# Kernel optimization log

Hardware: AMD Instinct MI355X
Metric: run time of the kernel (lower is better)

The kernel has to match this reference:

```python
import jax, jax.numpy as jnp
import numpy as np


def setup_inputs() -> dict:
    key = jax.random.key(0)
    k1, k2, k3 = jax.random.split(key, 3)
    B, T, C = 4, 2048, 1024
    x = jax.random.normal(k1, (B, T, C), dtype=jnp.float32)
    # Linear weights stored as (in, out) so y = x @ W + b
    w_attn = jax.random.normal(k2, (C, 3 * C), dtype=jnp.float32) * (1.0 / np.sqrt(C))
    b_attn = jnp.zeros((3 * C,), dtype=jnp.float32)
    w_proj = jax.random.normal(k3, (C, C), dtype=jnp.float32) * (1.0 / np.sqrt(C))
    b_proj = jnp.zeros((C,), dtype=jnp.float32)
    return {"x": x, "w_attn": w_attn, "b_attn": b_attn, "w_proj": w_proj, "b_proj": b_proj}


def reference(x, w_attn, b_attn, w_proj, b_proj):
    B, T, C = x.shape
    n_head = 16
    hd = C // n_head  # head dim = 64
    qkv = x @ w_attn + b_attn  # [B, T, 3C]
    q, k, v = jnp.split(qkv, 3, axis=-1)
    # [B, H, T, hd]
    q = q.reshape(B, T, n_head, hd).transpose(0, 2, 1, 3)
    k = k.reshape(B, T, n_head, hd).transpose(0, 2, 1, 3)
    v = v.reshape(B, T, n_head, hd).transpose(0, 2, 1, 3)
    scale = 1.0 / np.sqrt(hd).astype(np.float32)
    att = jnp.einsum("bhqd,bhkd->bhqk", q, k) * scale  # [B, H, T, T]
    causal = jnp.tril(jnp.ones((T, T), dtype=bool))
    att = jnp.where(causal[None, None], att, jnp.float32(-jnp.inf))
    att = jax.nn.softmax(att, axis=-1)
    y = jnp.einsum("bhqk,bhkd->bhqd", att, v)  # [B, H, T, hd]
    y = y.transpose(0, 2, 1, 3).reshape(B, T, C)
    return y @ w_proj + b_proj
```

## Files before the change

kernel.cpp:

```cpp
#include <hip/hip_runtime.h>

typedef __attribute__((ext_vector_type(8))) short short8;
typedef __attribute__((ext_vector_type(4))) float f32x4;
typedef unsigned short u16;
typedef unsigned int u32;

__device__ __forceinline__ float bf2f(u16 u) {
    union { u32 i; float f; } x;
    x.i = ((u32)u) << 16;
    return x.f;
}

__device__ __forceinline__ u16 f2bf(float f) {
    union { float f; u32 i; } x;
    x.f = f;
    u32 r = x.i + 0x7fffu + ((x.i >> 16) & 1u);
    return (u16)(r >> 16);
}

__global__ __launch_bounds__(256) void convert_bf16(const float* __restrict__ in,
                                                    u16* __restrict__ out) {
    const long i = ((long)blockIdx.x * 256 + threadIdx.x) * 8;
    f32x4 v0 = *(const f32x4*)(in + i);
    f32x4 v1 = *(const f32x4*)(in + i + 4);
    short8 o;
#pragma unroll
    for (int j = 0; j < 4; ++j) o[j] = (short)f2bf(v0[j]);
#pragma unroll
    for (int j = 0; j < 4; ++j) o[4 + j] = (short)f2bf(v1[j]);
    *(short8*)(out + i) = o;
}

__global__ __launch_bounds__(256) void transpose_f32_bf16(const float* __restrict__ in,
                                                          u16* __restrict__ out,
                                                          int K, int N) {
    __shared__ float tile[32][33];
    const int nb = blockIdx.x * 32, kb = blockIdx.y * 32;
    const int tx = threadIdx.x, ty = threadIdx.y;
#pragma unroll
    for (int i = 0; i < 32; i += 8)
        tile[ty + i][tx] = in[(long)(kb + ty + i) * N + nb + tx];
    __syncthreads();
#pragma unroll
    for (int i = 0; i < 32; i += 8)
        out[(long)(nb + ty + i) * K + kb + tx] = f2bf(tile[tx][ty + i]);
}

__global__ __launch_bounds__(256) void transpose_v(const u16* __restrict__ qkv,
                                                   u16* __restrict__ vT) {
    __shared__ u16 tile[32][33];
    const int tb = blockIdx.x * 32;
    const int db = blockIdx.y * 32;
    const int bh = blockIdx.z;
    const int b = bh >> 4, h = bh & 15;
    const int tx = threadIdx.x, ty = threadIdx.y;
#pragma unroll
    for (int i = 0; i < 32; i += 8)
        tile[ty + i][tx] = qkv[((long)b * 2048 + tb + ty + i) * 3072 + 2048 + h * 64 + db + tx];
    __syncthreads();
#pragma unroll
    for (int i = 0; i < 32; i += 8)
        vT[((long)bh * 64 + db + ty + i) * 2048 + tb + tx] = tile[tx][ty + i];
}

__global__ __launch_bounds__(256, 2) void gemm_bf16_bt(
    const u16* __restrict__ A, int lda, const u16* __restrict__ BT,
    const float* __restrict__ bias, u16* __restrict__ C,
    int M, int N, int K) {
    __shared__ u16 As[128 * 32];
    __shared__ u16 Bs[128 * 32];
    const int tid = threadIdx.x;
    const int wv = tid >> 6, lane = tid & 63, quad = lane >> 4, L = lane & 15;
    const int wm = (wv >> 1) * 64, wn = (wv & 1) * 64;
    const long m0 = (long)blockIdx.y * 128;
    const long n0 = (long)blockIdx.x * 128;

    const u16* Ag = A + (m0 + wv * 32 + (lane >> 2)) * (long)lda + (lane & 3) * 8;
    const u16* Bg = BT + (n0 + wv * 32 + (lane >> 2)) * (long)K + (lane & 3) * 8;
    u16* AsW = &As[wv * 32 * 32];
    u16* BsW = &Bs[wv * 32 * 32];

    f32x4 zero4 = {0.f, 0.f, 0.f, 0.f};
    f32x4 acc[4][4];
#pragma unroll
    for (int i = 0; i < 4; ++i)
#pragma unroll
        for (int j = 0; j < 4; ++j) acc[i][j] = zero4;

    for (int kb = 0; kb < K; kb += 32) {
        short8 a0 = *(const short8*)(Ag + kb);
        short8 a1 = *(const short8*)(Ag + kb + (long)16 * lda);
        short8 b0 = *(const short8*)(Bg + kb);
        short8 b1 = *(const short8*)(Bg + kb + (long)16 * K);
        __syncthreads();
        *(short8*)(AsW + lane * 8) = a0;
        *(short8*)(AsW + 512 + lane * 8) = a1;
        *(short8*)(BsW + lane * 8) = b0;
        *(short8*)(BsW + 512 + lane * 8) = b1;
        __syncthreads();

        short8 af[4], bf[4];
#pragma unroll
        for (int mt = 0; mt < 4; ++mt)
            af[mt] = *(const short8*)&As[(wm + mt * 16 + L) * 32 + quad * 8];
#pragma unroll
        for (int nt = 0; nt < 4; ++nt)
            bf[nt] = *(const short8*)&Bs[(wn + nt * 16 + L) * 32 + quad * 8];
#pragma unroll
        for (int mt = 0; mt < 4; ++mt)
#pragma unroll
            for (int nt = 0; nt < 4; ++nt)
                acc[mt][nt] = __builtin_amdgcn_mfma_f32_16x16x32_bf16(
                    af[mt], bf[nt], acc[mt][nt], 0, 0, 0);
    }

#pragma unroll
    for (int nt = 0; nt < 4; ++nt) {
        const long col = n0 + wn + nt * 16 + L;
        const float bv = bias[col];
#pragma unroll
        for (int mt = 0; mt < 4; ++mt)
#pragma unroll
            for (int r = 0; r < 4; ++r) {
                const long row = m0 + wm + mt * 16 + quad * 4 + r;
                C[row * N + col] = f2bf(acc[mt][nt][r] + bv);
            }
    }
}

__global__ __launch_bounds__(256, 2) void gemm_bf16_bn(
    const u16* __restrict__ A, int lda, const float* __restrict__ B,
    const float* __restrict__ bias, float* __restrict__ C,
    int M, int N, int K) {
    __shared__ u16 As[128 * 32];
    __shared__ u16 Bs[128 * 32];
    const int tid = threadIdx.x;
    const int wv = tid >> 6, lane = tid & 63, quad = lane >> 4, L = lane & 15;
    const int wm = (wv >> 1) * 64, wn = (wv & 1) * 64;
    const long m0 = (long)blockIdx.y * 128;
    const long n0 = (long)blockIdx.x * 128;

    const u16* Ag = A + (m0 + wv * 32 + (lane >> 2)) * (long)lda + (lane & 3) * 8;
    u16* AsW = &As[wv * 32 * 32];

    f32x4 zero4 = {0.f, 0.f, 0.f, 0.f};
    f32x4 acc[4][4];
#pragma unroll
    for (int i = 0; i < 4; ++i)
#pragma unroll
        for (int j = 0; j < 4; ++j) acc[i][j] = zero4;

    for (int kb = 0; kb < K; kb += 32) {
        short8 a0 = *(const short8*)(Ag + kb);
        short8 a1 = *(const short8*)(Ag + kb + (long)16 * lda);
        short8 p[2];
#pragma unroll
        for (int i = 0; i < 2; ++i) {
            const int c = tid + i * 256;
            const int n = c >> 2, k8 = (c & 3) * 8;
            const float* bp = B + (long)(kb + k8) * N + n0 + n;
#pragma unroll
            for (int j = 0; j < 8; ++j) p[i][j] = (short)f2bf(bp[(long)j * N]);
        }
        __syncthreads();
        *(short8*)(AsW + lane * 8) = a0;
        *(short8*)(AsW + 512 + lane * 8) = a1;
        *(short8*)(&Bs[tid * 8]) = p[0];
        *(short8*)(&Bs[(tid + 256) * 8]) = p[1];
        __syncthreads();

        short8 af[4], bf[4];
#pragma unroll
        for (int mt = 0; mt < 4; ++mt)
            af[mt] = *(const short8*)&As[(wm + mt * 16 + L) * 32 + quad * 8];
#pragma unroll
        for (int nt = 0; nt < 4; ++nt)
            bf[nt] = *(const short8*)&Bs[(wn + nt * 16 + L) * 32 + quad * 8];
#pragma unroll
        for (int mt = 0; mt < 4; ++mt)
#pragma unroll
            for (int nt = 0; nt < 4; ++nt)
                acc[mt][nt] = __builtin_amdgcn_mfma_f32_16x16x32_bf16(
                    af[mt], bf[nt], acc[mt][nt], 0, 0, 0);
    }

#pragma unroll
    for (int nt = 0; nt < 4; ++nt) {
        const long col = n0 + wn + nt * 16 + L;
        const float bv = bias[col];
#pragma unroll
        for (int mt = 0; mt < 4; ++mt)
#pragma unroll
            for (int r = 0; r < 4; ++r) {
                const long row = m0 + wm + mt * 16 + quad * 4 + r;
                C[row * N + col] = acc[mt][nt][r] + bv;
            }
    }
}

#define AT_T 2048

__global__ __launch_bounds__(256) void attn_kernel(u16* __restrict__ qkv,
                                                   const u16* __restrict__ vT) {
    __shared__ u16 Kt[2][32 * 72];
    __shared__ u16 Vt[2][64 * 40];
    __shared__ u16 Ps[4][16 * 72];
    const int tid = threadIdx.x;
    const int wv = tid >> 6, lane = tid & 63, quad = lane >> 4, L = lane & 15;
    const int bh = blockIdx.x;
    const int b = bh >> 4, h = bh & 15;
    const long rowbase = (long)b * AT_T;
    const long cbase = (long)h * 64;

    const int krow = tid >> 3, kc = tid & 7;
    const int vrow = tid >> 2, vc = tid & 3;
    const u16* Kg = qkv + (rowbase + krow) * 3072 + 1024 + cbase + kc * 8;
    const u16* Vg = vT + ((long)bh * 64 + vrow) * 2048 + vc * 8;

    short8 ones;
#pragma unroll
    for (int j = 0; j < 8; ++j) ones[j] = (L == 0) ? (short)0x3F80 : (short)0;

    f32x4 zero4 = {0.f, 0.f, 0.f, 0.f};
    u16* PsW = Ps[wv];

    for (int pass = 0; pass < 2; ++pass) {
        const int qtile = (pass == 0) ? (31 - (int)blockIdx.y) : (int)blockIdx.y;
        const int q0 = qtile * 64;
        const int qw0 = q0 + wv * 16;
        const int nkb = 2 * qtile + 2;

        short8 qf[2];
#pragma unroll
        for (int s = 0; s < 2; ++s)
            qf[s] = *(const short8*)&qkv[(rowbase + qw0 + L) * 3072 + cbase + s * 32 + quad * 8];

        f32x4 accO[4], accL = zero4;
#pragma unroll
        for (int nt = 0; nt < 4; ++nt) accO[nt] = zero4;

        {
            short8 k0r = *(const short8*)Kg;
            short8 v0r = *(const short8*)Vg;
            *(short8*)&Kt[0][krow * 72 + kc * 8] = k0r;
            *(short8*)&Vt[0][vrow * 40 + vc * 8] = v0r;
        }
        __syncthreads();

        int p = 0;
        for (int kb = 0; kb < nkb; ++kb) {
            const int k0 = kb * 32;
            const bool more = (kb + 1) < nkb;
            short8 knx, vnx;
            if (more) {
                knx = *(const short8*)(Kg + (long)(k0 + 32) * 3072);
                vnx = *(const short8*)(Vg + k0 + 32);
            }

            if (k0 <= qw0 + 15) {
                f32x4 sA[2];
#pragma unroll
                for (int nt = 0; nt < 2; ++nt) {
                    short8 kf0 = *(const short8*)&Kt[p][(nt * 16 + L) * 72 + quad * 8];
                    short8 kf1 = *(const short8*)&Kt[p][(nt * 16 + L) * 72 + 32 + quad * 8];
                    f32x4 z = __builtin_amdgcn_mfma_f32_16x16x32_bf16(qf[0], kf0, zero4, 0, 0, 0);
                    sA[nt] = __builtin_amdgcn_mfma_f32_16x16x32_bf16(qf[1], kf1, z, 0, 0, 0);
                }
                if (k0 + 31 > qw0) {
#pragma unroll
                    for (int nt = 0; nt < 2; ++nt) {
                        const int key = k0 + nt * 16 + L;
#pragma unroll
                        for (int r = 0; r < 4; ++r) {
                            const int qq = qw0 + quad * 4 + r;
                            const float v = (key <= qq) ? fmaf(sA[nt][r], 0.125f, -20.0f) : -1e30f;
                            PsW[(quad * 4 + r) * 72 + nt * 16 + L] =
                                (u16)(__float_as_uint(__expf(v)) >> 16);
                        }
                    }
                } else {
#pragma unroll
                    for (int nt = 0; nt < 2; ++nt)
#pragma unroll
                        for (int r = 0; r < 4; ++r) {
                            const float pv = __expf(fmaf(sA[nt][r], 0.125f, -20.0f));
                            PsW[(quad * 4 + r) * 72 + nt * 16 + L] =
                                (u16)(__float_as_uint(pv) >> 16);
                        }
                }
                short8 pf = *(const short8*)&PsW[L * 72 + quad * 8];
                accL = __builtin_amdgcn_mfma_f32_16x16x32_bf16(pf, ones, accL, 0, 0, 0);
#pragma unroll
                for (int nt = 0; nt < 4; ++nt) {
                    short8 vf = *(const short8*)&Vt[p][(nt * 16 + L) * 40 + quad * 8];
                    accO[nt] = __builtin_amdgcn_mfma_f32_16x16x32_bf16(pf, vf, accO[nt], 0, 0, 0);
                }
            }

            if (more) {
                *(short8*)&Kt[p ^ 1][krow * 72 + kc * 8] = knx;
                *(short8*)&Vt[p ^ 1][vrow * 40 + vc * 8] = vnx;
            }
            __syncthreads();
            p ^= 1;
        }

#pragma unroll
        for (int r = 0; r < 4; ++r) {
            const float l = __shfl(accL[r], lane & 48);
            const float inv = 1.f / l;
            const long orow = (rowbase + qw0 + quad * 4 + r) * 3072 + cbase;
#pragma unroll
            for (int nt = 0; nt < 4; ++nt)
                qkv[orow + nt * 16 + L] = f2bf(accO[nt][r] * inv);
        }
    }
}

extern "C" void kernel_launch(void* const* d_in, const int* in_sizes, int n_in,
                              void* d_out, int out_size, void* d_ws, size_t ws_size,
                              hipStream_t stream) {
    const float* x      = (const float*)d_in[0];
    const float* w_attn = (const float*)d_in[1];
    const float* b_attn = (const float*)d_in[2];
    const float* w_proj = (const float*)d_in[3];
    const float* b_proj = (const float*)d_in[4];
    float* out = (float*)d_out;

    u16* qkv = (u16*)d_ws;
    u16* xb  = (u16*)d_out;
    u16* wTa = (u16*)((char*)d_out + 16777216);
    u16* vT  = (u16*)d_out;

    convert_bf16<<<4096, 256, 0, stream>>>(x, xb);
    transpose_f32_bf16<<<dim3(3072 / 32, 1024 / 32), dim3(32, 8), 0, stream>>>(
        w_attn, wTa, 1024, 3072);
    gemm_bf16_bt<<<dim3(3072 / 128, 8192 / 128), 256, 0, stream>>>(
        xb, 1024, wTa, b_attn, qkv, 8192, 3072, 1024);
    transpose_v<<<dim3(64, 2, 64), dim3(32, 8), 0, stream>>>(qkv, vT);
    attn_kernel<<<dim3(64, 16), 256, 0, stream>>>(qkv, vT);
    gemm_bf16_bn<<<dim3(1024 / 128, 8192 / 128), 256, 0, stream>>>(
        qkv, 3072, w_proj, b_proj, out, 8192, 1024, 1024);
}
```

Measured before the change: 296.6 us.

## Use 32x32x16 MFMA with register-resident P in attention kernel

The attention kernel moves from 16x16x32 to 32x32x16 MFMA tiles and computes S transposed (K as the A operand), so each lane already holds probabilities in the layout the PV MFMA needs. P is packed with v_cvt_pk_bf16 and rearranged with permlane32 swaps instead of a round trip through shared memory, and exp is computed with exp2 using pre-folded constants. Query tiles grow to 128 rows with 32 rows per wave, which halves the grid. The cost is coarser causal-skip granularity, fewer blocks, and higher register pressure from the 16-wide accumulators.

```diff
diff --git a/kernel.cpp b/kernel.cpp
--- a/kernel.cpp
+++ b/kernel.cpp
@@ -2,6 +2,7 @@
 
 typedef __attribute__((ext_vector_type(8))) short short8;
 typedef __attribute__((ext_vector_type(4))) float f32x4;
+typedef __attribute__((ext_vector_type(16))) float f32x16;
 typedef unsigned short u16;
 typedef unsigned int u32;
 
@@ -17,6 +18,32 @@
     u32 r = x.i + 0x7fffu + ((x.i >> 16) & 1u);
     return (u16)(r >> 16);
 }
+
+__device__ __forceinline__ u32 cvt_pk_bf16(float lo, float hi) {
+    u32 d;
+    asm("v_cvt_pk_bf16_f32 %0, %1, %2" : "=v"(d) : "v"(lo), "v"(hi));
+    return d;
+}
+
+__device__ __forceinline__ void pswap(u32& a, u32& b) {
+#if __has_builtin(__builtin_amdgcn_permlane32_swap)
+    auto r = __builtin_amdgcn_permlane32_swap(a, b, false, false);
+    a = r[0];
+    b = r[1];
+#else
+    const int l = (int)(threadIdx.x & 63);
+    const u32 ax = __shfl(a, l ^ 32);
+    const u32 bx = __shfl(b, l ^ 32);
+    a = (l < 32) ? a : bx;
+    b = (l < 32) ? ax : b;
+#endif
+}
+
+#if __has_builtin(__builtin_amdgcn_exp2f)
+#define EXP2F(x) __builtin_amdgcn_exp2f(x)
+#else
+#define EXP2F(x) exp2f(x)
+#endif
 
 __global__ __launch_bounds__(256) void convert_bf16(const float* __restrict__ in,
                                                     u16* __restrict__ out) {
@@ -204,9 +231,9 @@
                                                    const u16* __restrict__ vT) {
     __shared__ u16 Kt[2][32 * 72];
     __shared__ u16 Vt[2][64 * 40];
-    __shared__ u16 Ps[4][16 * 72];
     const int tid = threadIdx.x;
-    const int wv = tid >> 6, lane = tid & 63, quad = lane >> 4, L = lane & 15;
+    const int wv = tid >> 6, lane = tid & 63;
+    const int hi = lane >> 5, cc = lane & 31;
     const int bh = blockIdx.x;
     const int b = bh >> 4, h = bh & 15;
     const long rowbase = (long)b * AT_T;
@@ -219,25 +246,25 @@
 
     short8 ones;
 #pragma unroll
-    for (int j = 0; j < 8; ++j) ones[j] = (L == 0) ? (short)0x3F80 : (short)0;
-
-    f32x4 zero4 = {0.f, 0.f, 0.f, 0.f};
-    u16* PsW = Ps[wv];
+    for (int j = 0; j < 8; ++j) ones[j] = (cc == 0) ? (short)0x3F80 : (short)0;
+
+    const float C1 = 0.18033688f;
+    const float C0 = -28.8539008f;
 
     for (int pass = 0; pass < 2; ++pass) {
-        const int qtile = (pass == 0) ? (31 - (int)blockIdx.y) : (int)blockIdx.y;
-        const int q0 = qtile * 64;
-        const int qw0 = q0 + wv * 16;
-        const int nkb = 2 * qtile + 2;
-
-        short8 qf[2];
-#pragma unroll
-        for (int s = 0; s < 2; ++s)
-            qf[s] = *(const short8*)&qkv[(rowbase + qw0 + L) * 3072 + cbase + s * 32 + quad * 8];
-
-        f32x4 accO[4], accL = zero4;
-#pragma unroll
-        for (int nt = 0; nt < 4; ++nt) accO[nt] = zero4;
+        const int qt = (pass == 0) ? (15 - (int)blockIdx.y) : (int)blockIdx.y;
+        const int q0 = qt * 128;
+        const int qw = q0 + wv * 32;
+        const int nkb = 4 * qt + 4;
+
+        short8 qf[4];
+#pragma unroll
+        for (int ks = 0; ks < 4; ++ks)
+            qf[ks] = *(const short8*)&qkv[(rowbase + qw + cc) * 3072 + cbase + ks * 16 + hi * 8];
+
+        f32x16 accO0, accO1, accL;
+#pragma unroll
+        for (int r = 0; r < 16; ++r) { accO0[r] = 0.f; accO1[r] = 0.f; accL[r] = 0.f; }
 
         {
             short8 k0r = *(const short8*)Kg;
@@ -257,43 +284,50 @@
                 vnx = *(const short8*)(Vg + k0 + 32);
             }
 
-            if (k0 <= qw0 + 15) {
-                f32x4 sA[2];
-#pragma unroll
-                for (int nt = 0; nt < 2; ++nt) {
-                    short8 kf0 = *(const short8*)&Kt[p][(nt * 16 + L) * 72 + quad * 8];
-                    short8 kf1 = *(const short8*)&Kt[p][(nt * 16 + L) * 72 + 32 + quad * 8];
-                    f32x4 z = __builtin_amdgcn_mfma_f32_16x16x32_bf16(qf[0], kf0, zero4, 0, 0, 0);
-                    sA[nt] = __builtin_amdgcn_mfma_f32_16x16x32_bf16(qf[1], kf1, z, 0, 0, 0);
+            if (k0 <= qw) {
+                f32x16 s;
+#pragma unroll
+                for (int r = 0; r < 16; ++r) s[r] = 0.f;
+#pragma unroll
+                for (int ks = 0; ks < 4; ++ks) {
+                    short8 kf = *(const short8*)&Kt[p][cc * 72 + ks * 16 + hi * 8];
+                    s = __builtin_amdgcn_mfma_f32_32x32x16_bf16(kf, qf[ks], s, 0, 0, 0);
                 }
-                if (k0 + 31 > qw0) {
-#pragma unroll
-                    for (int nt = 0; nt < 2; ++nt) {
-                        const int key = k0 + nt * 16 + L;
-#pragma unroll
-                        for (int r = 0; r < 4; ++r) {
-                            const int qq = qw0 + quad * 4 + r;
-                            const float v = (key <= qq) ? fmaf(sA[nt][r], 0.125f, -20.0f) : -1e30f;
-                            PsW[(quad * 4 + r) * 72 + nt * 16 + L] =
-                                (u16)(__float_as_uint(__expf(v)) >> 16);
-                        }
+                float pe[16];
+                if (k0 == qw) {
+#pragma unroll
+                    for (int r = 0; r < 16; ++r) {
+                        const int key = (r & 3) + 8 * (r >> 2) + 4 * hi;
+                        const float e = EXP2F(fmaf(s[r], C1, C0));
+                        pe[r] = (key <= cc) ? e : 0.f;
                     }
                 } else {
 #pragma unroll
-                    for (int nt = 0; nt < 2; ++nt)
-#pragma unroll
-                        for (int r = 0; r < 4; ++r) {
-                            const float pv = __expf(fmaf(sA[nt][r], 0.125f, -20.0f));
-                            PsW[(quad * 4 + r) * 72 + nt * 16 + L] =
-                                (u16)(__float_as_uint(pv) >> 16);
-                        }
+                    for (int r = 0; r < 16; ++r) pe[r] = EXP2F(fmaf(s[r], C1, C0));
                 }
-                short8 pf = *(const short8*)&PsW[L * 72 + quad * 8];
-                accL = __builtin_amdgcn_mfma_f32_16x16x32_bf16(pf, ones, accL, 0, 0, 0);
-#pragma unroll
-                for (int nt = 0; nt < 4; ++nt) {
-                    short8 vf = *(const short8*)&Vt[p][(nt * 16 + L) * 40 + quad * 8];
-                    accO[nt] = __builtin_amdgcn_mfma_f32_16x16x32_bf16(pf, vf, accO[nt], 0, 0, 0);
+
+                short8 pa[2];
+#pragma unroll
+                for (int ks = 0; ks < 2; ++ks) {
+                    u32 wA = cvt_pk_bf16(pe[8 * ks + 0], pe[8 * ks + 1]);
+                    u32 wB = cvt_pk_bf16(pe[8 * ks + 2], pe[8 * ks + 3]);
+                    u32 wC = cvt_pk_bf16(pe[8 * ks + 4], pe[8 * ks + 5]);
+                    u32 wD = cvt_pk_bf16(pe[8 * ks + 6], pe[8 * ks + 7]);
+                    pswap(wA, wC);
+                    pswap(wB, wD);
+                    union { u32 d[4]; short8 v; } u;
+                    u.d[0] = wA; u.d[1] = wB; u.d[2] = wC; u.d[3] = wD;
+                    pa[ks] = u.v;
+                }
+
+                accL = __builtin_amdgcn_mfma_f32_32x32x16_bf16(pa[0], ones, accL, 0, 0, 0);
+                accL = __builtin_amdgcn_mfma_f32_32x32x16_bf16(pa[1], ones, accL, 0, 0, 0);
+#pragma unroll
+                for (int ks = 0; ks < 2; ++ks) {
+                    short8 vf0 = *(const short8*)&Vt[p][cc * 40 + ks * 16 + hi * 8];
+                    short8 vf1 = *(const short8*)&Vt[p][(32 + cc) * 40 + ks * 16 + hi * 8];
+                    accO0 = __builtin_amdgcn_mfma_f32_32x32x16_bf16(pa[ks], vf0, accO0, 0, 0, 0);
+                    accO1 = __builtin_amdgcn_mfma_f32_32x32x16_bf16(pa[ks], vf1, accO1, 0, 0, 0);
                 }
             }
 
@@ -306,13 +340,13 @@
         }
 
 #pragma unroll
-        for (int r = 0; r < 4; ++r) {
-            const float l = __shfl(accL[r], lane & 48);
+        for (int r = 0; r < 16; ++r) {
+            const float l = __shfl(accL[r], lane & 32);
             const float inv = 1.f / l;
-            const long orow = (rowbase + qw0 + quad * 4 + r) * 3072 + cbase;
-#pragma unroll
-            for (int nt = 0; nt < 4; ++nt)
-                qkv[orow + nt * 16 + L] = f2bf(accO[nt][r] * inv);
+            const int q = (r & 3) + 8 * (r >> 2) + 4 * hi;
+            const long orow = (rowbase + qw + q) * 3072 + cbase;
+            qkv[orow + cc] = f2bf(accO0[r] * inv);
+            qkv[orow + 32 + cc] = f2bf(accO1[r] * inv);
         }
     }
 }
@@ -338,7 +372,7 @@
     gemm_bf16_bt<<<dim3(3072 / 128, 8192 / 128), 256, 0, stream>>>(
         xb, 1024, wTa, b_attn, qkv, 8192, 3072, 1024);
     transpose_v<<<dim3(64, 2, 64), dim3(32, 8), 0, stream>>>(qkv, vT);
-    attn_kernel<<<dim3(64, 16), 256, 0, stream>>>(qkv, vT);
+    attn_kernel<<<dim3(64, 8), 256, 0, stream>>>(qkv, vT);
     gemm_bf16_bn<<<dim3(1024 / 128, 8192 / 128), 256, 0, stream>>>(
         qkv, 3072, w_proj, b_proj, out, 8192, 1024, 1024);
 }
```

After: 298.2 us. Within noise of the previous version (+0.6%).
